# Kernel tuning notes

Measured on AMD Instinct MI355X. Metric: run time of the kernel, lower is better.

Reference implementation:

```python
import jax, jax.numpy as jnp
import numpy as np

B = 262144
INPUT_DIM = 4
NUM_STEPS = 50          # int(0.5 / 0.01)
H = 0.01                # time_step
SIGMA, RHO, BETA = 10.0, 28.0, 8.0 / 3.0
COUPLING_STRENGTH = 1.0


def _xavier(key, fan_in, fan_out):
    limit = float(np.sqrt(6.0 / (fan_in + fan_out)))
    return jax.random.uniform(key, (fan_in, fan_out), jnp.float32, -limit, limit)


def setup_inputs() -> dict:
    key = jax.random.key(0)
    ks = jax.random.split(key, 7)
    features = jax.random.normal(ks[0], (B, INPUT_DIM), jnp.float32)
    return {
        "features": features,
        # initial_state_mapper: Linear(4,16) -> tanh -> Linear(16,3) -> tanh
        "W1": _xavier(ks[1], INPUT_DIM, 16), "b1": jnp.zeros((16,), jnp.float32),
        "W2": _xavier(ks[2], 16, 3),         "b2": jnp.zeros((3,), jnp.float32),
        # coupling_mapper: Linear(4,8) -> tanh -> Linear(8,3) -> tanh
        "Wc1": _xavier(ks[3], INPUT_DIM, 8), "bc1": jnp.zeros((8,), jnp.float32),
        "Wc2": _xavier(ks[4], 8, 3),         "bc2": jnp.zeros((3,), jnp.float32),
        # param_adapter: Linear(4,8) -> relu -> Linear(8,3) -> sigmoid
        "Wp1": _xavier(ks[5], INPUT_DIM, 8), "bp1": jnp.zeros((8,), jnp.float32),
        "Wp2": _xavier(ks[6], 8, 3),         "bp2": jnp.zeros((3,), jnp.float32),
    }


def _lorenz(state, coupling, params):
    x, y, z = state[:, 0], state[:, 1], state[:, 2]
    s, r, b = params[:, 0], params[:, 1], params[:, 2]
    dx = s * (y - x) + coupling[:, 0]
    dy = x * (r - z) - y + coupling[:, 1]
    dz = x * y - b * z + coupling[:, 2]
    return jnp.stack([dx, dy, dz], axis=1)


def _rk4(state, coupling, params):
    k1 = _lorenz(state, coupling, params)
    k2 = _lorenz(state + 0.5 * H * k1, coupling, params)
    k3 = _lorenz(state + 0.5 * H * k2, coupling, params)
    k4 = _lorenz(state + H * k3, coupling, params)
    return state + (H / 6.0) * (k1 + 2.0 * k2 + 2.0 * k3 + k4)


def reference(features, W1, b1, W2, b2, Wc1, bc1, Wc2, bc2, Wp1, bp1, Wp2, bp2):
    # initial states, scaled by 2
    init = jnp.tanh(jnp.tanh(features @ W1 + b1) @ W2 + b2) * 2.0
    # couplings
    coup = jnp.tanh(jnp.tanh(features @ Wc1 + bc1) @ Wc2 + bc2) * COUPLING_STRENGTH
    # adapted lorenz parameters
    scales = jax.nn.sigmoid(jax.nn.relu(features @ Wp1 + bp1) @ Wp2 + bp2)
    params = jnp.stack([
        SIGMA * (0.5 + scales[:, 0]),
        RHO * (0.5 + scales[:, 1]),
        BETA * (0.5 + scales[:, 2]),
    ], axis=1)

    def step(state, _):
        nxt = _rk4(state, coup, params)
        return nxt, nxt

    _, traj = jax.lax.scan(step, init, None, length=NUM_STEPS - 1)  # [T-1, B, 3]
    traj = jnp.concatenate([init[None], traj], axis=0)              # [T, B, 3]
    return jnp.transpose(traj, (1, 0, 2))                           # [B, T, 3]
```

## Files before the change

kernel.cpp:

```cpp
#include <hip/hip_runtime.h>

#define NSTEP 50
#define ROWW 75

__device__ __forceinline__ void lorenz(float x, float y, float z,
                                       float S, float R, float Bb,
                                       float c0, float c1, float c2,
                                       float& dx, float& dy, float& dz) {
    dx = S * (y - x) + c0;
    dy = x * (R - z) - y + c1;
    dz = x * y - Bb * z + c2;
}

__device__ __forceinline__ unsigned int bpack(float lo, float hi) {
    unsigned int a = (__builtin_bit_cast(unsigned int, lo) + 0x8000u) >> 16;
    unsigned int b = (__builtin_bit_cast(unsigned int, hi) + 0x8000u) & 0xFFFF0000u;
    return a | b;
}
__device__ __forceinline__ float bunpack_lo(unsigned int w) {
    return __builtin_bit_cast(float, w << 16);
}
__device__ __forceinline__ float bunpack_hi(unsigned int w) {
    return __builtin_bit_cast(float, w & 0xFFFF0000u);
}

__device__ __forceinline__ float tanh_fast(float x) {
    float e = __expf(2.0f * x);
    float r = __builtin_amdgcn_rcpf(e + 1.0f);
    return __builtin_fmaf(-2.0f, r, 1.0f);
}
__device__ __forceinline__ float sigmoid_fast(float x) {
    float e = __expf(-x);
    return __builtin_amdgcn_rcpf(1.0f + e);
}

__global__ __launch_bounds__(64) void chaotic_embed_kernel(
    const float* __restrict__ features,
    const float* __restrict__ W1,  const float* __restrict__ b1,
    const float* __restrict__ W2,  const float* __restrict__ b2,
    const float* __restrict__ Wc1, const float* __restrict__ bc1,
    const float* __restrict__ Wc2, const float* __restrict__ bc2,
    const float* __restrict__ Wp1, const float* __restrict__ bp1,
    const float* __restrict__ Wp2, const float* __restrict__ bp2,
    float* __restrict__ out)
{
    __shared__ unsigned int img[64 * ROWW];
    const int lane = threadIdx.x;
    const long p = (long)blockIdx.x * 64 + lane;

    const float4 f4 = ((const float4*)features)[p];
    const float fv[4] = {f4.x, f4.y, f4.z, f4.w};

    float h1[16];
    #pragma unroll
    for (int j = 0; j < 16; ++j) {
        float a = b1[j];
        #pragma unroll
        for (int i = 0; i < 4; ++i) a = __builtin_fmaf(fv[i], W1[i * 16 + j], a);
        h1[j] = tanh_fast(a);
    }
    float init[3];
    #pragma unroll
    for (int c = 0; c < 3; ++c) {
        float a = b2[c];
        #pragma unroll
        for (int j = 0; j < 16; ++j) a = __builtin_fmaf(h1[j], W2[j * 3 + c], a);
        init[c] = 2.0f * tanh_fast(a);
    }
    float hc[8];
    #pragma unroll
    for (int j = 0; j < 8; ++j) {
        float a = bc1[j];
        #pragma unroll
        for (int i = 0; i < 4; ++i) a = __builtin_fmaf(fv[i], Wc1[i * 8 + j], a);
        hc[j] = tanh_fast(a);
    }
    float coup[3];
    #pragma unroll
    for (int c = 0; c < 3; ++c) {
        float a = bc2[c];
        #pragma unroll
        for (int j = 0; j < 8; ++j) a = __builtin_fmaf(hc[j], Wc2[j * 3 + c], a);
        coup[c] = tanh_fast(a);
    }
    float hp[8];
    #pragma unroll
    for (int j = 0; j < 8; ++j) {
        float a = bp1[j];
        #pragma unroll
        for (int i = 0; i < 4; ++i) a = __builtin_fmaf(fv[i], Wp1[i * 8 + j], a);
        hp[j] = fmaxf(a, 0.0f);
    }
    float sc[3];
    #pragma unroll
    for (int c = 0; c < 3; ++c) {
        float a = bp2[c];
        #pragma unroll
        for (int j = 0; j < 8; ++j) a = __builtin_fmaf(hp[j], Wp2[j * 3 + c], a);
        sc[c] = sigmoid_fast(a);
    }
    const float S  = 10.0f * (0.5f + sc[0]);
    const float R  = 28.0f * (0.5f + sc[1]);
    const float Bb = (8.0f / 3.0f) * (0.5f + sc[2]);
    const float c0 = coup[0], c1 = coup[1], c2 = coup[2];
    const float H = 0.01f, HH = 0.5f * 0.01f, H6 = 0.01f / 6.0f;

    float sx = init[0], sy = init[1], sz = init[2];
    float px = sx, py = sy, pz = sz;

    unsigned int* row = img + lane * ROWW;

    int u = 0;
    #pragma unroll 2
    for (int t = 1; t < NSTEP; ++t) {
        float k1x, k1y, k1z, k2x, k2y, k2z, k3x, k3y, k3z, k4x, k4y, k4z;
        lorenz(sx, sy, sz, S, R, Bb, c0, c1, c2, k1x, k1y, k1z);
        lorenz(sx + HH * k1x, sy + HH * k1y, sz + HH * k1z,
               S, R, Bb, c0, c1, c2, k2x, k2y, k2z);
        lorenz(sx + HH * k2x, sy + HH * k2y, sz + HH * k2z,
               S, R, Bb, c0, c1, c2, k3x, k3y, k3z);
        lorenz(sx + H * k3x, sy + H * k3y, sz + H * k3z,
               S, R, Bb, c0, c1, c2, k4x, k4y, k4z);
        sx += H6 * (k1x + 2.0f * k2x + 2.0f * k3x + k4x);
        sy += H6 * (k1y + 2.0f * k2y + 2.0f * k3y + k4y);
        sz += H6 * (k1z + 2.0f * k2z + 2.0f * k3z + k4z);

        if (t & 1) {
            row[u + 0] = bpack(px, py);
            row[u + 1] = bpack(pz, sx);
            row[u + 2] = bpack(sy, sz);
            u += 3;
        } else {
            px = sx; py = sy; pz = sz;
        }
    }

    __syncthreads();

    float4* __restrict__ outv = (float4*)(out + (long)blockIdx.x * (64 * 150));
    const uint2* __restrict__ img2 = (const uint2*)img;
    for (int g = lane; g < 2400; g += 64) {
        const uint2 ww = img2[g];
        float4 v;
        v.x = bunpack_lo(ww.x);
        v.y = bunpack_hi(ww.x);
        v.z = bunpack_lo(ww.y);
        v.w = bunpack_hi(ww.y);
        outv[g] = v;
    }
}

extern "C" void kernel_launch(void* const* d_in, const int* in_sizes, int n_in,
                              void* d_out, int out_size, void* d_ws, size_t ws_size,
                              hipStream_t stream) {
    const float* features = (const float*)d_in[0];
    const float* W1  = (const float*)d_in[1];
    const float* b1  = (const float*)d_in[2];
    const float* W2  = (const float*)d_in[3];
    const float* b2  = (const float*)d_in[4];
    const float* Wc1 = (const float*)d_in[5];
    const float* bc1 = (const float*)d_in[6];
    const float* Wc2 = (const float*)d_in[7];
    const float* bc2 = (const float*)d_in[8];
    const float* Wp1 = (const float*)d_in[9];
    const float* bp1 = (const float*)d_in[10];
    const float* Wp2 = (const float*)d_in[11];
    const float* bp2 = (const float*)d_in[12];
    float* out = (float*)d_out;

    const int B = in_sizes[0] / 4;
    const int grid = B / 64;

    chaotic_embed_kernel<<<grid, 64, 0, stream>>>(
        features, W1, b1, W2, b2, Wc1, bc1, Wc2, bc2,
        Wp1, bp1, Wp2, bp2, out);
}
```

Baseline: 46.81 us.

## Flush trajectory in staggered chunks to overlap stores with RK4 compute

Replaces the single full-trajectory LDS image plus final write-out with a small per-lane buffer that is flushed to global memory every few time steps. The first chunk length varies per block (hashed from the block id), so different blocks issue their stores at different times and memory traffic spreads across the run instead of bursting at the end. This shrinks LDS use, which may allow higher occupancy. The costs are extra flush calls with less coalesced float2 stores and a data-dependent switch. There is also no barrier between the LDS writes and the cross-lane reads, which relies on the 64-thread block being a single wavefront.

```diff
diff --git a/kernel.cpp b/kernel.cpp
--- a/kernel.cpp
+++ b/kernel.cpp
@@ -1,7 +1,7 @@
 #include <hip/hip_runtime.h>
 
 #define NSTEP 50
-#define ROWW 75
+#define STR 21
 
 __device__ __forceinline__ void lorenz(float x, float y, float z,
                                        float S, float R, float Bb,
@@ -32,6 +32,23 @@
 __device__ __forceinline__ float sigmoid_fast(float x) {
     float e = __expf(-x);
     return __builtin_amdgcn_rcpf(1.0f + e);
+}
+
+template<int CNT>
+__device__ __forceinline__ void flushT(const unsigned int* __restrict__ fb,
+                                       float* __restrict__ outW,
+                                       int lane, int e0dw) {
+    #pragma unroll
+    for (int k = 0; k < CNT; ++k) {
+        const int i  = 64 * k + lane;
+        const int pp = i / CNT;
+        const int j  = i - pp * CNT;
+        const unsigned int v = fb[pp * STR + j];
+        float2 o;
+        o.x = bunpack_lo(v);
+        o.y = bunpack_hi(v);
+        *(float2*)(outW + pp * 150 + e0dw + 2 * j) = o;
+    }
 }
 
 __global__ __launch_bounds__(64) void chaotic_embed_kernel(
@@ -44,9 +61,11 @@
     const float* __restrict__ Wp2, const float* __restrict__ bp2,
     float* __restrict__ out)
 {
-    __shared__ unsigned int img[64 * ROWW];
+    __shared__ unsigned int buf[64 * STR];
+
     const int lane = threadIdx.x;
-    const long p = (long)blockIdx.x * 64 + lane;
+    const int bid  = blockIdx.x;
+    const long p   = (long)bid * 64 + lane;
 
     const float4 f4 = ((const float4*)features)[p];
     const float fv[4] = {f4.x, f4.y, f4.z, f4.w};
@@ -106,13 +125,9 @@
     const float H = 0.01f, HH = 0.5f * 0.01f, H6 = 0.01f / 6.0f;
 
     float sx = init[0], sy = init[1], sz = init[2];
-    float px = sx, py = sy, pz = sz;
-
-    unsigned int* row = img + lane * ROWW;
-
-    int u = 0;
-    #pragma unroll 2
-    for (int t = 1; t < NSTEP; ++t) {
+    float px, py, pz;
+
+    auto step = [&]() {
         float k1x, k1y, k1z, k2x, k2y, k2z, k3x, k3y, k3z, k4x, k4y, k4z;
         lorenz(sx, sy, sz, S, R, Bb, c0, c1, c2, k1x, k1y, k1z);
         lorenz(sx + HH * k1x, sy + HH * k1y, sz + HH * k1z,
@@ -124,29 +139,38 @@
         sx += H6 * (k1x + 2.0f * k2x + 2.0f * k3x + k4x);
         sy += H6 * (k1y + 2.0f * k2y + 2.0f * k3y + k4y);
         sz += H6 * (k1z + 2.0f * k2z + 2.0f * k3z + k4z);
-
-        if (t & 1) {
+    };
+
+    unsigned int* row = buf + lane * STR;
+    float* __restrict__ outW = out + (long)bid * (64 * 150);
+
+    const int variant = (bid ^ (bid >> 2) ^ (bid >> 8)) & 3;
+
+    int e   = 0;
+    int len = 6 + 2 * variant;
+    while (e < NSTEP) {
+        if (len > NSTEP - e) len = NSTEP - e;
+        const int len2 = len >> 1;
+        int u = 0;
+        for (int g = 0; g < len2; ++g) {
+            if (e + 2 * g > 0) step();
+            px = sx; py = sy; pz = sz;
+            step();
             row[u + 0] = bpack(px, py);
             row[u + 1] = bpack(pz, sx);
             row[u + 2] = bpack(sy, sz);
             u += 3;
-        } else {
-            px = sx; py = sy; pz = sz;
         }
-    }
-
-    __syncthreads();
-
-    float4* __restrict__ outv = (float4*)(out + (long)blockIdx.x * (64 * 150));
-    const uint2* __restrict__ img2 = (const uint2*)img;
-    for (int g = lane; g < 2400; g += 64) {
-        const uint2 ww = img2[g];
-        float4 v;
-        v.x = bunpack_lo(ww.x);
-        v.y = bunpack_hi(ww.x);
-        v.z = bunpack_lo(ww.y);
-        v.w = bunpack_hi(ww.y);
-        outv[g] = v;
+        switch (len2) {
+            case 6:  flushT<18>(buf, outW, lane, 3 * e); break;
+            case 5:  flushT<15>(buf, outW, lane, 3 * e); break;
+            case 4:  flushT<12>(buf, outW, lane, 3 * e); break;
+            case 3:  flushT< 9>(buf, outW, lane, 3 * e); break;
+            case 2:  flushT< 6>(buf, outW, lane, 3 * e); break;
+            default: flushT< 3>(buf, outW, lane, 3 * e); break;
+        }
+        e += len;
+        len = 12;
     }
 }
 
```

Measured after the change: 61.46 us. 31.3% more time.

## Split block into producer and consumer waves with LDS flag handoff

Applied to the files above, without the earlier changes.

Each 512-thread block now has 4 compute waves that integrate two 64-row batches each into per-wave LDS slots, and 4 store waves that copy finished slots to global memory. The two sides hand off through spin-waited ready/freed flags in LDS. The aim is to overlap trajectory computation with the global stores, which previously ran one after the other inside each 64-thread block. The cost is half the waves sitting idle in spin loops, a bounded spin guard that could break correctness if it times out, and the compute waves stalling until their slot is freed before starting the second batch.

```diff
diff --git a/kernel.cpp b/kernel.cpp
--- a/kernel.cpp
+++ b/kernel.cpp
@@ -1,7 +1,9 @@
 #include <hip/hip_runtime.h>
 
+#define NT 512
 #define NSTEP 50
 #define ROWW 75
+#define SLOT (64 * ROWW)
 
 __device__ __forceinline__ void lorenz(float x, float y, float z,
                                        float S, float R, float Bb,
@@ -34,7 +36,15 @@
     return __builtin_amdgcn_rcpf(1.0f + e);
 }
 
-__global__ __launch_bounds__(64) void chaotic_embed_kernel(
+__device__ __forceinline__ void waitGE(const int* f, int v) {
+    int guard = 0;
+    while (*(const volatile int*)f < v) {
+        __builtin_amdgcn_s_sleep(2);
+        if (++guard > (1 << 20)) break;
+    }
+}
+
+__global__ __launch_bounds__(NT) void chaotic_embed_kernel(
     const float* __restrict__ features,
     const float* __restrict__ W1,  const float* __restrict__ b1,
     const float* __restrict__ W2,  const float* __restrict__ b2,
@@ -44,109 +54,145 @@
     const float* __restrict__ Wp2, const float* __restrict__ bp2,
     float* __restrict__ out)
 {
-    __shared__ unsigned int img[64 * ROWW];
-    const int lane = threadIdx.x;
-    const long p = (long)blockIdx.x * 64 + lane;
-
-    const float4 f4 = ((const float4*)features)[p];
-    const float fv[4] = {f4.x, f4.y, f4.z, f4.w};
-
-    float h1[16];
-    #pragma unroll
-    for (int j = 0; j < 16; ++j) {
-        float a = b1[j];
-        #pragma unroll
-        for (int i = 0; i < 4; ++i) a = __builtin_fmaf(fv[i], W1[i * 16 + j], a);
-        h1[j] = tanh_fast(a);
-    }
-    float init[3];
-    #pragma unroll
-    for (int c = 0; c < 3; ++c) {
-        float a = b2[c];
-        #pragma unroll
-        for (int j = 0; j < 16; ++j) a = __builtin_fmaf(h1[j], W2[j * 3 + c], a);
-        init[c] = 2.0f * tanh_fast(a);
-    }
-    float hc[8];
-    #pragma unroll
-    for (int j = 0; j < 8; ++j) {
-        float a = bc1[j];
-        #pragma unroll
-        for (int i = 0; i < 4; ++i) a = __builtin_fmaf(fv[i], Wc1[i * 8 + j], a);
-        hc[j] = tanh_fast(a);
-    }
-    float coup[3];
-    #pragma unroll
-    for (int c = 0; c < 3; ++c) {
-        float a = bc2[c];
-        #pragma unroll
-        for (int j = 0; j < 8; ++j) a = __builtin_fmaf(hc[j], Wc2[j * 3 + c], a);
-        coup[c] = tanh_fast(a);
-    }
-    float hp[8];
-    #pragma unroll
-    for (int j = 0; j < 8; ++j) {
-        float a = bp1[j];
-        #pragma unroll
-        for (int i = 0; i < 4; ++i) a = __builtin_fmaf(fv[i], Wp1[i * 8 + j], a);
-        hp[j] = fmaxf(a, 0.0f);
-    }
-    float sc[3];
-    #pragma unroll
-    for (int c = 0; c < 3; ++c) {
-        float a = bp2[c];
-        #pragma unroll
-        for (int j = 0; j < 8; ++j) a = __builtin_fmaf(hp[j], Wp2[j * 3 + c], a);
-        sc[c] = sigmoid_fast(a);
-    }
-    const float S  = 10.0f * (0.5f + sc[0]);
-    const float R  = 28.0f * (0.5f + sc[1]);
-    const float Bb = (8.0f / 3.0f) * (0.5f + sc[2]);
-    const float c0 = coup[0], c1 = coup[1], c2 = coup[2];
-    const float H = 0.01f, HH = 0.5f * 0.01f, H6 = 0.01f / 6.0f;
-
-    float sx = init[0], sy = init[1], sz = init[2];
-    float px = sx, py = sy, pz = sz;
-
-    unsigned int* row = img + lane * ROWW;
-
-    int u = 0;
-    #pragma unroll 2
-    for (int t = 1; t < NSTEP; ++t) {
-        float k1x, k1y, k1z, k2x, k2y, k2z, k3x, k3y, k3z, k4x, k4y, k4z;
-        lorenz(sx, sy, sz, S, R, Bb, c0, c1, c2, k1x, k1y, k1z);
-        lorenz(sx + HH * k1x, sy + HH * k1y, sz + HH * k1z,
-               S, R, Bb, c0, c1, c2, k2x, k2y, k2z);
-        lorenz(sx + HH * k2x, sy + HH * k2y, sz + HH * k2z,
-               S, R, Bb, c0, c1, c2, k3x, k3y, k3z);
-        lorenz(sx + H * k3x, sy + H * k3y, sz + H * k3z,
-               S, R, Bb, c0, c1, c2, k4x, k4y, k4z);
-        sx += H6 * (k1x + 2.0f * k2x + 2.0f * k3x + k4x);
-        sy += H6 * (k1y + 2.0f * k2y + 2.0f * k3y + k4y);
-        sz += H6 * (k1z + 2.0f * k2z + 2.0f * k3z + k4z);
-
-        if (t & 1) {
-            row[u + 0] = bpack(px, py);
-            row[u + 1] = bpack(pz, sx);
-            row[u + 2] = bpack(sy, sz);
-            u += 3;
-        } else {
-            px = sx; py = sy; pz = sz;
+    __shared__ unsigned int stage[4 * SLOT];
+    __shared__ int ready[4];
+    __shared__ int freed[4];
+
+    const int tid  = threadIdx.x;
+    const int wv   = tid >> 6;
+    const int lane = tid & 63;
+    const int w    = wv & 3;
+
+    if (tid < 4) { ready[tid] = 0; freed[tid] = 0; }
+    __syncthreads();
+
+    const long blockBase = (long)blockIdx.x * 512;
+
+    if (wv < 4) {
+        unsigned int* row = stage + w * SLOT + lane * ROWW;
+
+        for (int s = 0; s < 2; ++s) {
+            if (s == 1) waitGE(&freed[w], 1);
+
+            const long p = blockBase + (long)w * 128 + (long)s * 64 + lane;
+            const float4 f4 = ((const float4*)features)[p];
+            const float fv[4] = {f4.x, f4.y, f4.z, f4.w};
+
+            float h1[16];
+            #pragma unroll
+            for (int j = 0; j < 16; ++j) {
+                float a = b1[j];
+                #pragma unroll
+                for (int i = 0; i < 4; ++i) a = __builtin_fmaf(fv[i], W1[i * 16 + j], a);
+                h1[j] = tanh_fast(a);
+            }
+            float init[3];
+            #pragma unroll
+            for (int c = 0; c < 3; ++c) {
+                float a = b2[c];
+                #pragma unroll
+                for (int j = 0; j < 16; ++j) a = __builtin_fmaf(h1[j], W2[j * 3 + c], a);
+                init[c] = 2.0f * tanh_fast(a);
+            }
+            float hc[8];
+            #pragma unroll
+            for (int j = 0; j < 8; ++j) {
+                float a = bc1[j];
+                #pragma unroll
+                for (int i = 0; i < 4; ++i) a = __builtin_fmaf(fv[i], Wc1[i * 8 + j], a);
+                hc[j] = tanh_fast(a);
+            }
+            float coup[3];
+            #pragma unroll
+            for (int c = 0; c < 3; ++c) {
+                float a = bc2[c];
+                #pragma unroll
+                for (int j = 0; j < 8; ++j) a = __builtin_fmaf(hc[j], Wc2[j * 3 + c], a);
+                coup[c] = tanh_fast(a);
+            }
+            float hp[8];
+            #pragma unroll
+            for (int j = 0; j < 8; ++j) {
+                float a = bp1[j];
+                #pragma unroll
+                for (int i = 0; i < 4; ++i) a = __builtin_fmaf(fv[i], Wp1[i * 8 + j], a);
+                hp[j] = fmaxf(a, 0.0f);
+            }
+            float sc[3];
+            #pragma unroll
+            for (int c = 0; c < 3; ++c) {
+                float a = bp2[c];
+                #pragma unroll
+                for (int j = 0; j < 8; ++j) a = __builtin_fmaf(hp[j], Wp2[j * 3 + c], a);
+                sc[c] = sigmoid_fast(a);
+            }
+            const float S  = 10.0f * (0.5f + sc[0]);
+            const float R  = 28.0f * (0.5f + sc[1]);
+            const float Bb = (8.0f / 3.0f) * (0.5f + sc[2]);
+            const float c0 = coup[0], c1 = coup[1], c2 = coup[2];
+            const float H = 0.01f, HH = 0.5f * 0.01f, H6 = 0.01f / 6.0f;
+
+            float sx = init[0], sy = init[1], sz = init[2];
+            float px = sx, py = sy, pz = sz;
+
+            int u = 0;
+            #pragma unroll 2
+            for (int t = 1; t < NSTEP; ++t) {
+                float k1x, k1y, k1z, k2x, k2y, k2z, k3x, k3y, k3z, k4x, k4y, k4z;
+                lorenz(sx, sy, sz, S, R, Bb, c0, c1, c2, k1x, k1y, k1z);
+                lorenz(sx + HH * k1x, sy + HH * k1y, sz + HH * k1z,
+                       S, R, Bb, c0, c1, c2, k2x, k2y, k2z);
+                lorenz(sx + HH * k2x, sy + HH * k2y, sz + HH * k2z,
+                       S, R, Bb, c0, c1, c2, k3x, k3y, k3z);
+                lorenz(sx + H * k3x, sy + H * k3y, sz + H * k3z,
+                       S, R, Bb, c0, c1, c2, k4x, k4y, k4z);
+                sx += H6 * (k1x + 2.0f * k2x + 2.0f * k3x + k4x);
+                sy += H6 * (k1y + 2.0f * k2y + 2.0f * k3y + k4y);
+                sz += H6 * (k1z + 2.0f * k2z + 2.0f * k3z + k4z);
+
+                if (t & 1) {
+                    row[u + 0] = bpack(px, py);
+                    row[u + 1] = bpack(pz, sx);
+                    row[u + 2] = bpack(sy, sz);
+                    u += 3;
+                } else {
+                    px = sx; py = sy; pz = sz;
+                }
+            }
+
+            __threadfence_block();
+            if (lane == 0) *(volatile int*)&ready[w] = s + 1;
         }
-    }
-
-    __syncthreads();
-
-    float4* __restrict__ outv = (float4*)(out + (long)blockIdx.x * (64 * 150));
-    const uint2* __restrict__ img2 = (const uint2*)img;
-    for (int g = lane; g < 2400; g += 64) {
-        const uint2 ww = img2[g];
-        float4 v;
-        v.x = bunpack_lo(ww.x);
-        v.y = bunpack_hi(ww.x);
-        v.z = bunpack_lo(ww.y);
-        v.w = bunpack_hi(ww.y);
-        outv[g] = v;
+    } else {
+        const uint2* __restrict__ img2 = (const uint2*)(stage + w * SLOT);
+
+        for (int s = 0; s < 2; ++s) {
+            waitGE(&ready[w], s + 1);
+
+            uint2 pr[38];
+            #pragma unroll
+            for (int k = 0; k < 38; ++k) {
+                const int g = 64 * k + lane;
+                if (k < 37 || lane < 32) pr[k] = img2[g];
+            }
+            __threadfence_block();
+            if (lane == 0) *(volatile int*)&freed[w] = s + 1;
+
+            float4* __restrict__ outv = (float4*)(out +
+                (blockBase + (long)w * 128 + (long)s * 64) * (3 * NSTEP));
+            #pragma unroll
+            for (int k = 0; k < 38; ++k) {
+                const int g = 64 * k + lane;
+                if (k < 37 || lane < 32) {
+                    float4 v;
+                    v.x = bunpack_lo(pr[k].x);
+                    v.y = bunpack_hi(pr[k].x);
+                    v.z = bunpack_lo(pr[k].y);
+                    v.w = bunpack_hi(pr[k].y);
+                    outv[g] = v;
+                }
+            }
+        }
     }
 }
 
@@ -169,9 +215,9 @@
     float* out = (float*)d_out;
 
     const int B = in_sizes[0] / 4;
-    const int grid = B / 64;
-
-    chaotic_embed_kernel<<<grid, 64, 0, stream>>>(
+    const int grid = B / 512;
+
+    chaotic_embed_kernel<<<grid, NT, 0, stream>>>(
         features, W1, b1, W2, b2, Wc1, bc1, Wc2, bc2,
         Wp1, bp1, Wp2, bp2, out);
 }
```

Measured after the change: 50.66 us. 8.2% more time.

## Process two row batches per block, reusing one LDS tile with wave-level fences

Applied to the files above, without the earlier changes.

Each 64-thread block now handles two batches of 64 rows in sequence, reusing a single LDS staging tile. The __syncthreads is replaced by s_waitcnt lgkmcnt fences, since the block is one wavefront. The integration loop is restructured into paired steps so packing happens without a branch, and the store loop is unrolled with a fixed trip count. This halves the grid and amortises block launch and weight loads, at the cost of serialising the second batch's compute after the first batch's stores.

```diff
diff --git a/kernel.cpp b/kernel.cpp
--- a/kernel.cpp
+++ b/kernel.cpp
@@ -1,7 +1,9 @@
 #include <hip/hip_runtime.h>
 
 #define NSTEP 50
+#define RND 2
 #define ROWW 75
+#define NT 64
 
 __device__ __forceinline__ void lorenz(float x, float y, float z,
                                        float S, float R, float Bb,
@@ -34,7 +36,11 @@
     return __builtin_amdgcn_rcpf(1.0f + e);
 }
 
-__global__ __launch_bounds__(64) void chaotic_embed_kernel(
+__device__ __forceinline__ void lds_fence() {
+    asm volatile("s_waitcnt lgkmcnt(0)" ::: "memory");
+}
+
+__global__ __launch_bounds__(NT, 2) void chaotic_embed_kernel(
     const float* __restrict__ features,
     const float* __restrict__ W1,  const float* __restrict__ b1,
     const float* __restrict__ W2,  const float* __restrict__ b2,
@@ -44,109 +50,127 @@
     const float* __restrict__ Wp2, const float* __restrict__ bp2,
     float* __restrict__ out)
 {
-    __shared__ unsigned int img[64 * ROWW];
+    __shared__ unsigned int tile[NT * ROWW];
     const int lane = threadIdx.x;
-    const long p = (long)blockIdx.x * 64 + lane;
-
-    const float4 f4 = ((const float4*)features)[p];
-    const float fv[4] = {f4.x, f4.y, f4.z, f4.w};
-
-    float h1[16];
-    #pragma unroll
-    for (int j = 0; j < 16; ++j) {
-        float a = b1[j];
-        #pragma unroll
-        for (int i = 0; i < 4; ++i) a = __builtin_fmaf(fv[i], W1[i * 16 + j], a);
-        h1[j] = tanh_fast(a);
-    }
-    float init[3];
-    #pragma unroll
-    for (int c = 0; c < 3; ++c) {
-        float a = b2[c];
-        #pragma unroll
-        for (int j = 0; j < 16; ++j) a = __builtin_fmaf(h1[j], W2[j * 3 + c], a);
-        init[c] = 2.0f * tanh_fast(a);
-    }
-    float hc[8];
-    #pragma unroll
-    for (int j = 0; j < 8; ++j) {
-        float a = bc1[j];
-        #pragma unroll
-        for (int i = 0; i < 4; ++i) a = __builtin_fmaf(fv[i], Wc1[i * 8 + j], a);
-        hc[j] = tanh_fast(a);
-    }
-    float coup[3];
-    #pragma unroll
-    for (int c = 0; c < 3; ++c) {
-        float a = bc2[c];
-        #pragma unroll
-        for (int j = 0; j < 8; ++j) a = __builtin_fmaf(hc[j], Wc2[j * 3 + c], a);
-        coup[c] = tanh_fast(a);
-    }
-    float hp[8];
-    #pragma unroll
-    for (int j = 0; j < 8; ++j) {
-        float a = bp1[j];
-        #pragma unroll
-        for (int i = 0; i < 4; ++i) a = __builtin_fmaf(fv[i], Wp1[i * 8 + j], a);
-        hp[j] = fmaxf(a, 0.0f);
-    }
-    float sc[3];
-    #pragma unroll
-    for (int c = 0; c < 3; ++c) {
-        float a = bp2[c];
-        #pragma unroll
-        for (int j = 0; j < 8; ++j) a = __builtin_fmaf(hp[j], Wp2[j * 3 + c], a);
-        sc[c] = sigmoid_fast(a);
-    }
-    const float S  = 10.0f * (0.5f + sc[0]);
-    const float R  = 28.0f * (0.5f + sc[1]);
-    const float Bb = (8.0f / 3.0f) * (0.5f + sc[2]);
-    const float c0 = coup[0], c1 = coup[1], c2 = coup[2];
-    const float H = 0.01f, HH = 0.5f * 0.01f, H6 = 0.01f / 6.0f;
-
-    float sx = init[0], sy = init[1], sz = init[2];
-    float px = sx, py = sy, pz = sz;
-
-    unsigned int* row = img + lane * ROWW;
-
-    int u = 0;
-    #pragma unroll 2
-    for (int t = 1; t < NSTEP; ++t) {
-        float k1x, k1y, k1z, k2x, k2y, k2z, k3x, k3y, k3z, k4x, k4y, k4z;
-        lorenz(sx, sy, sz, S, R, Bb, c0, c1, c2, k1x, k1y, k1z);
-        lorenz(sx + HH * k1x, sy + HH * k1y, sz + HH * k1z,
-               S, R, Bb, c0, c1, c2, k2x, k2y, k2z);
-        lorenz(sx + HH * k2x, sy + HH * k2y, sz + HH * k2z,
-               S, R, Bb, c0, c1, c2, k3x, k3y, k3z);
-        lorenz(sx + H * k3x, sy + H * k3y, sz + H * k3z,
-               S, R, Bb, c0, c1, c2, k4x, k4y, k4z);
-        sx += H6 * (k1x + 2.0f * k2x + 2.0f * k3x + k4x);
-        sy += H6 * (k1y + 2.0f * k2y + 2.0f * k3y + k4y);
-        sz += H6 * (k1z + 2.0f * k2z + 2.0f * k3z + k4z);
-
-        if (t & 1) {
-            row[u + 0] = bpack(px, py);
-            row[u + 1] = bpack(pz, sx);
-            row[u + 2] = bpack(sy, sz);
-            u += 3;
-        } else {
+    const long pbase = (long)blockIdx.x * (NT * RND);
+
+    const float4 f40 = ((const float4*)features)[pbase + lane];
+    const float4 f41 = ((const float4*)features)[pbase + NT + lane];
+
+    unsigned int* row = tile + lane * ROWW;
+
+    for (int r = 0; r < RND; ++r) {
+        const float4 f4 = r ? f41 : f40;
+        const float fv[4] = {f4.x, f4.y, f4.z, f4.w};
+
+        float h1[16];
+        #pragma unroll
+        for (int j = 0; j < 16; ++j) {
+            float a = b1[j];
+            #pragma unroll
+            for (int i = 0; i < 4; ++i) a = __builtin_fmaf(fv[i], W1[i * 16 + j], a);
+            h1[j] = tanh_fast(a);
+        }
+        float init[3];
+        #pragma unroll
+        for (int c = 0; c < 3; ++c) {
+            float a = b2[c];
+            #pragma unroll
+            for (int j = 0; j < 16; ++j) a = __builtin_fmaf(h1[j], W2[j * 3 + c], a);
+            init[c] = 2.0f * tanh_fast(a);
+        }
+        float hc[8];
+        #pragma unroll
+        for (int j = 0; j < 8; ++j) {
+            float a = bc1[j];
+            #pragma unroll
+            for (int i = 0; i < 4; ++i) a = __builtin_fmaf(fv[i], Wc1[i * 8 + j], a);
+            hc[j] = tanh_fast(a);
+        }
+        float coup[3];
+        #pragma unroll
+        for (int c = 0; c < 3; ++c) {
+            float a = bc2[c];
+            #pragma unroll
+            for (int j = 0; j < 8; ++j) a = __builtin_fmaf(hc[j], Wc2[j * 3 + c], a);
+            coup[c] = tanh_fast(a);
+        }
+        float hp[8];
+        #pragma unroll
+        for (int j = 0; j < 8; ++j) {
+            float a = bp1[j];
+            #pragma unroll
+            for (int i = 0; i < 4; ++i) a = __builtin_fmaf(fv[i], Wp1[i * 8 + j], a);
+            hp[j] = fmaxf(a, 0.0f);
+        }
+        float sc[3];
+        #pragma unroll
+        for (int c = 0; c < 3; ++c) {
+            float a = bp2[c];
+            #pragma unroll
+            for (int j = 0; j < 8; ++j) a = __builtin_fmaf(hp[j], Wp2[j * 3 + c], a);
+            sc[c] = sigmoid_fast(a);
+        }
+        const float S  = 10.0f * (0.5f + sc[0]);
+        const float R  = 28.0f * (0.5f + sc[1]);
+        const float Bb = (8.0f / 3.0f) * (0.5f + sc[2]);
+        const float c0 = coup[0], c1 = coup[1], c2 = coup[2];
+        const float H = 0.01f, HH = 0.5f * 0.01f, H6 = 0.01f / 6.0f;
+
+        float sx = init[0], sy = init[1], sz = init[2];
+        float px, py, pz;
+
+        auto step = [&]() {
+            float k1x, k1y, k1z, k2x, k2y, k2z, k3x, k3y, k3z, k4x, k4y, k4z;
+            lorenz(sx, sy, sz, S, R, Bb, c0, c1, c2, k1x, k1y, k1z);
+            lorenz(sx + HH * k1x, sy + HH * k1y, sz + HH * k1z,
+                   S, R, Bb, c0, c1, c2, k2x, k2y, k2z);
+            lorenz(sx + HH * k2x, sy + HH * k2y, sz + HH * k2z,
+                   S, R, Bb, c0, c1, c2, k3x, k3y, k3z);
+            lorenz(sx + H * k3x, sy + H * k3y, sz + H * k3z,
+                   S, R, Bb, c0, c1, c2, k4x, k4y, k4z);
+            sx += H6 * (k1x + 2.0f * k2x + 2.0f * k3x + k4x);
+            sy += H6 * (k1y + 2.0f * k2y + 2.0f * k3y + k4y);
+            sz += H6 * (k1z + 2.0f * k2z + 2.0f * k3z + k4z);
+        };
+
+        {
             px = sx; py = sy; pz = sz;
-        }
-    }
-
-    __syncthreads();
-
-    float4* __restrict__ outv = (float4*)(out + (long)blockIdx.x * (64 * 150));
-    const uint2* __restrict__ img2 = (const uint2*)img;
-    for (int g = lane; g < 2400; g += 64) {
-        const uint2 ww = img2[g];
-        float4 v;
-        v.x = bunpack_lo(ww.x);
-        v.y = bunpack_hi(ww.x);
-        v.z = bunpack_lo(ww.y);
-        v.w = bunpack_hi(ww.y);
-        outv[g] = v;
+            step();
+            row[0] = bpack(px, py);
+            row[1] = bpack(pz, sx);
+            row[2] = bpack(sy, sz);
+        }
+        #pragma unroll 2
+        for (int g = 1; g < 25; ++g) {
+            step();
+            px = sx; py = sy; pz = sz;
+            step();
+            row[3 * g + 0] = bpack(px, py);
+            row[3 * g + 1] = bpack(pz, sx);
+            row[3 * g + 2] = bpack(sy, sz);
+        }
+
+        lds_fence();
+
+        float4* __restrict__ outv =
+            (float4*)out + (long)blockIdx.x * (RND * 2400) + r * 2400;
+        const uint2* __restrict__ img2 = (const uint2*)tile;
+        #pragma unroll 4
+        for (int k = 0; k < 38; ++k) {
+            const int i = 64 * k + lane;
+            if (k < 37 || lane < 32) {
+                const uint2 ww = img2[i];
+                float4 v;
+                v.x = bunpack_lo(ww.x);
+                v.y = bunpack_hi(ww.x);
+                v.z = bunpack_lo(ww.y);
+                v.w = bunpack_hi(ww.y);
+                outv[i] = v;
+            }
+        }
+
+        lds_fence();
     }
 }
 
@@ -169,9 +193,9 @@
     float* out = (float*)d_out;
 
     const int B = in_sizes[0] / 4;
-    const int grid = B / 64;
-
-    chaotic_embed_kernel<<<grid, 64, 0, stream>>>(
+    const int grid = B / (NT * RND);
+
+    chaotic_embed_kernel<<<grid, NT, 0, stream>>>(
         features, W1, b1, W2, b2, Wc1, bc1, Wc2, bc2,
         Wp1, bp1, Wp2, bp2, out);
 }
```

Result: slower. 51.63 us (+10.3%).
